# Optimization experiments

Measured on AMD Instinct MI355X. Metric: run time of the kernel, lower is better.

## Reference

```python
import jax, jax.numpy as jnp
import numpy as np

SIGMA = 1.0   # noise std (unit-variance synthetic input)
P = 11        # patch size p1
K = 16        # number of similar patches k1
WIN = 65      # search window w (odd)
S = 3         # reference-patch stride
ALPHA = 0.5   # n2n alpha


def _unfold(x, ksize, stride):
    # (N,1,H,W) -> (N, ksize*ksize, Ho, Wo); kernel positions row-major (== torch F.unfold for C=1)
    return jax.lax.conv_general_dilated_patches(
        x, (ksize, ksize), (stride, stride), 'VALID',
        dimension_numbers=('NCHW', 'OIHW', 'NCHW'))


def block_matching(x, k, p, w, s):
    N, _, H, W = x.shape
    v = w // 2
    assert (H - p + 1) % s == 1 and (W - p + 1) % s == 1  # no edge-case branches needed
    Href = (H - p) // s + 1
    Wref = (W - p) // s + 1
    x_pad = jnp.pad(x, ((0, 0), (0, 0), (v, v), (v, v)))  # zero pad; invalid candidates masked below
    # |patch|^2 / p^2 at every position of the padded image (== F.avg_pool2d(x**2, p))
    sq = jax.lax.reduce_window(x_pad * x_pad, 0.0, jax.lax.add,
                               (1, 1, p, p), (1, 1, 1, 1), 'VALID') / (p * p)
    norms = _unfold(sq, 2 * v + 1, s)                                  # (N,(2v+1)^2,Href,Wref)
    norms = norms.reshape(N, 2 * v + 1, 2 * v + 1, Href, Wref).transpose(0, 3, 4, 1, 2)
    lw = _unfold(x_pad, 2 * v + p, s) / p                              # (N,(2v+p)^2,Href,Wref)
    lw = lw.reshape(N, 2 * v + p, 2 * v + p, Href, Wref).transpose(0, 3, 4, 1, 2)
    G = N * Href * Wref
    lw = lw.reshape(1, G, 2 * v + p, 2 * v + p)
    ref = lw[0, :, v:-v, v:-v][:, None]                                # (G,1,p,p) reference patches
    sp = jax.lax.conv_general_dilated(
        lw, ref, (1, 1), 'VALID',
        dimension_numbers=('NCHW', 'OIHW', 'NCHW'),
        feature_group_count=G)                                         # (1,G,2v+1,2v+1)
    dist = norms.reshape(1, G, 2 * v + 1, 2 * v + 1) - 2.0 * sp
    dist = dist.reshape(N, Href, Wref, 2 * v + 1, 2 * v + 1)
    # mask candidate patches that fall outside the original image (torch uses NaN padding + topk)
    offs = jnp.arange(-v, v + 1)
    hr = jnp.arange(Href) * s
    wr = jnp.arange(Wref) * s
    row_ok = (hr[:, None] + offs >= 0) & (hr[:, None] + offs <= H - p)  # (Href, 2v+1)
    col_ok = (wr[:, None] + offs >= 0) & (wr[:, None] + offs <= W - p)  # (Wref, 2v+1)
    valid = row_ok[:, None, :, None] & col_ok[None, :, None, :]
    dist = jnp.where(valid[None], dist, jnp.inf)
    dist = dist.at[..., v, v].set(-jnp.inf)                            # reference patch always kept
    dist = dist.reshape(N, Href, Wref, (2 * v + 1) ** 2)
    _, idx = jax.lax.top_k(-dist, k)                                   # k smallest distances
    ind_row = idx // (2 * v + 1) - v
    ind_col = idx % (2 * v + 1) - v
    ind = (ind_row + hr[None, :, None, None]) * (W - p + 1) + (ind_col + wr[None, None, :, None])
    return ind.reshape(N, -1)                                          # (N, Href*Wref*k)


def gather_groups(y, indices, k, p):
    N = y.shape[0]
    uf = _unfold(y, p, 1).reshape(N, p * p, -1)                        # (N, n, (H-p+1)(W-p+1))
    Yg = jnp.take_along_axis(uf, indices[:, None, :], axis=2)          # (N, n, L*k)
    L = indices.shape[1] // k
    return Yg.reshape(N, p * p, L, k).transpose(0, 2, 3, 1)            # (N, L, k, n)


def denoise1(Y, sigma):
    # method='n2n', constraints='affine'
    N, B, k, n = Y.shape
    D = n * sigma ** 2
    E = n * ALPHA ** 2 * sigma ** 2
    Ik = jnp.eye(k, dtype=Y.dtype)
    Q = Y @ jnp.swapaxes(Y, 2, 3) + E * Ik                             # (N,B,k,k), SPD
    Lc = jnp.linalg.cholesky(Q)
    Ikb = jnp.broadcast_to(Ik, Q.shape)
    Z = jax.scipy.linalg.solve_triangular(Lc, Ikb, lower=True)
    Qinv = jax.scipy.linalg.solve_triangular(jnp.swapaxes(Lc, 2, 3), Z, lower=False)
    Qinv1 = jnp.sum(Qinv, axis=3, keepdims=True)
    Qinv2 = jnp.sum(Qinv1, axis=2, keepdims=True)
    theta = Ik - (Qinv - (Qinv1 @ jnp.swapaxes(Qinv1, 2, 3)) / Qinv2) * (D + E)
    theta = jnp.swapaxes(theta, 2, 3)
    X_hat = theta @ Y
    weights = 1.0 / jnp.clip(jnp.sum(theta * theta, axis=3, keepdims=True), 1.0 / k, 1.0)
    return X_hat, weights


def _fold(x, H, W, p):
    # inverse of unfold: sum overlapping p x p patches back onto the image grid
    N, n, _ = x.shape
    Hp, Wp = H - p + 1, W - p + 1
    x = x.reshape(N, p, p, Hp, Wp)
    out = jnp.zeros((N, 1, H, W), x.dtype)
    for a in range(p):
        for b in range(p):
            out = out.at[:, 0, a:a + Hp, b:b + Wp].add(x[:, a, b])
    return out


def aggregate(X_hat, weights, indices, H, W, p):
    N, L, k, n = X_hat.shape
    X = (X_hat * weights).reshape(N, L * k, n).transpose(0, 2, 1)      # (N, n, L*k)
    Wt = jnp.broadcast_to(weights, (N, L, k, n)).reshape(N, L * k, n).transpose(0, 2, 1)
    Lfull = (H - p + 1) * (W - p + 1)
    def scat(vals, idx):
        return jnp.zeros((n, Lfull), vals.dtype).at[:, idx].add(vals)
    X_sum = jax.vmap(scat)(X, indices)
    W_sum = jax.vmap(scat)(Wt, indices)
    return _fold(X_sum, H, W, p) / _fold(W_sum, H, W, p)


def _forward(y):
    N, C, H, W = y.shape
    indices = block_matching(y, K, P, WIN, S)
    Yg = gather_groups(y, indices, K, P)
    X_hat, weights = denoise1(Yg, SIGMA)
    return aggregate(X_hat, weights, indices, H, W, P)


def setup_inputs():
    key = jax.random.key(0)
    y = jax.random.normal(key, (4, 1, 128, 128), dtype=jnp.float32)
    return {"y": y}


def reference(y):
    return _forward(y)
```

## Files before the change

### kernel.cpp

```cpp
#include <hip/hip_runtime.h>
#include <math.h>

#define HH 128
#define WW 128
#define NIMG 4
#define PP 11
#define KSIM 16
#define STRIDE_S 3
#define VRAD 32
#define WINW 65
#define NTASK (WINW*9)
#define HREF 40
#define WREF 40
#define NPOS 118
#define WROWS 75
#define WPITCH 84
#define NGROUP (NIMG*HREF*WREF)
#define EPS_E 30.25f
#define DE_C 151.25f
#define INFD 3.0e38f
#define RTASK 292
#define THREC 152

__global__ __launch_bounds__(256, 6)
void bm_kernel(const float* __restrict__ y, int* __restrict__ inds)
{
    __shared__ float win[WROWS][WPITCH];
    __shared__ float swv[4];
    __shared__ int   swi[4];

    const int blk = blockIdx.x;
    const int n   = blk / (HREF*WREF);
    const int rem = blk % (HREF*WREF);
    const int hr  = (rem / WREF) * STRIDE_S;
    const int wr  = (rem % WREF) * STRIDE_S;
    const float* img = y + n * HH * WW;
    const int tid = threadIdx.x;

    for (int t = tid; t < WROWS * WPITCH; t += 256) {
        int r = t / WPITCH, c = t % WPITCH;
        int gr = hr - VRAD + r, gc = wr - VRAD + c;
        float v = 0.f;
        if (c < WROWS && gr >= 0 && gr < HH && gc >= 0 && gc < WW)
            v = img[gr * WW + gc];
        win[r][c] = v;
    }
    __syncthreads();

    float d[3][8];
#pragma unroll
    for (int s = 0; s < 3; s++)
#pragma unroll
        for (int c = 0; c < 8; c++) d[s][c] = INFD;

#pragma unroll
    for (int s = 0; s < 3; s++) {
        int task = tid + (s << 8);
        if (task < NTASK) {
            int drx = task % WINW;
            int c0  = (task / WINW) * 8;
            int rr  = hr + drx - VRAD;
            bool rowok = (rr >= 0 && rr <= HH - PP);
            if (rowok) {
                float dot[8];
                float colsq[18];
#pragma unroll
                for (int c = 0; c < 8; c++) dot[c] = 0.f;
#pragma unroll
                for (int j2 = 0; j2 < 18; j2++) colsq[j2] = 0.f;
                for (int a = 0; a < PP; a++) {
                    const float4* w4 = reinterpret_cast<const float4*>(&win[drx + a][c0]);
                    float4 A0 = w4[0], A1 = w4[1], A2 = w4[2], A3 = w4[3];
                    float2 A4 = *reinterpret_cast<const float2*>(&win[drx + a][c0 + 16]);
                    float wv[18] = {A0.x,A0.y,A0.z,A0.w, A1.x,A1.y,A1.z,A1.w,
                                    A2.x,A2.y,A2.z,A2.w, A3.x,A3.y,A3.z,A3.w,
                                    A4.x,A4.y};
                    const float4* r4 = reinterpret_cast<const float4*>(&win[VRAD + a][VRAD]);
                    float4 R0 = r4[0], R1 = r4[1];
                    float2 R2 = *reinterpret_cast<const float2*>(&win[VRAD + a][VRAD + 8]);
                    float  R3 = win[VRAD + a][VRAD + 10];
                    float rv[11] = {R0.x,R0.y,R0.z,R0.w, R1.x,R1.y,R1.z,R1.w,
                                    R2.x,R2.y, R3};
#pragma unroll
                    for (int j2 = 0; j2 < 18; j2++) colsq[j2] += wv[j2] * wv[j2];
#pragma unroll
                    for (int b = 0; b < PP; b++) {
#pragma unroll
                        for (int c = 0; c < 8; c++)
                            dot[c] += wv[b + c] * rv[b];
                    }
                }
#pragma unroll
                for (int j2 = 1; j2 < 18; j2++) colsq[j2] += colsq[j2 - 1];
#pragma unroll
                for (int c = 0; c < 8; c++) {
                    int dcx = c0 + c;
                    int cc  = wr + dcx - VRAD;
                    float norm = colsq[c + 10] - (c ? colsq[c - 1] : 0.f);
                    if (dcx < WINW && cc >= 0 && cc <= WW - PP)
                        d[s][c] = norm - 2.f * dot[c];
                }
            }
            if (task == RTASK) d[s][0] = -INFD;
        }
    }

    float lval = INFD; int lidx = 0;
#pragma unroll
    for (int s = 0; s < 3; s++)
#pragma unroll
        for (int c = 0; c < 8; c++)
            if (d[s][c] < lval) { lval = d[s][c]; lidx = (s << 3) | c; }

    for (int sel = 0; sel < KSIM; sel++) {
        float rv = lval;
        int   ri = ((tid + ((lidx >> 3) << 8)) << 3) | (lidx & 7);
#pragma unroll
        for (int off = 32; off > 0; off >>= 1) {
            float ov = __shfl_down(rv, off);
            int   oi = __shfl_down(ri, off);
            if (ov < rv) { rv = ov; ri = oi; }
        }
        if ((tid & 63) == 0) { swv[tid >> 6] = rv; swi[tid >> 6] = ri; }
        __syncthreads();
        float bval = swv[0]; int bidx = swi[0];
#pragma unroll
        for (int w2 = 1; w2 < 4; w2++)
            if (swv[w2] < bval) { bval = swv[w2]; bidx = swi[w2]; }
        if (tid == 0) {
            int task2 = bidx >> 3;
            int drx = task2 % WINW;
            int dcx = (task2 / WINW) * 8 + (bidx & 7);
            inds[blk * KSIM + sel] =
                (hr + drx - VRAD) * NPOS + (wr + dcx - VRAD);
        }
        __syncthreads();
        int otid = (bidx >> 3) & 255;
        if (tid == otid) {
            int code = (((bidx >> 3) >> 8) << 3) | (bidx & 7);
            lval = INFD; lidx = 0;
#pragma unroll
            for (int s = 0; s < 3; s++)
#pragma unroll
                for (int c = 0; c < 8; c++) {
                    if (((s << 3) | c) == code) d[s][c] = INFD;
                    if (d[s][c] < lval) { lval = d[s][c]; lidx = (s << 3) | c; }
                }
        }
    }
}

__global__ __launch_bounds__(256)
void dn_solve(const float* __restrict__ y, const int* __restrict__ inds,
              float* __restrict__ thW)
{
    __shared__ float Yp[4][16][124];
    __shared__ float Qs[4][16][17];
    __shared__ float s1[4][16];
    __shared__ float s2[4];
    __shared__ float wl[4][16];
    __shared__ short pr_[4][16], pc_[4][16];

    const int blk = blockIdx.x;
    const int tid = threadIdx.x;
    const int g0 = blk * 4;

    if (tid < 64) {
        int gq = tid >> 4, m = tid & 15;
        int idx = inds[(g0 + gq) * KSIM + m];
        pr_[gq][m] = (short)(idx / NPOS);
        pc_[gq][m] = (short)(idx % NPOS);
    }
    if (tid < 192) {
        int gq = tid / 48, m = (tid / 3) % 16, e = tid % 3;
        Yp[gq][m][121 + e] = 0.f;
    }
    __syncthreads();

    for (int t = tid; t < 4 * 16 * 121; t += 256) {
        int gq = t / 1936, m = (t / 121) % 16, j = t % 121;
        int a = j / PP, b = j % PP;
        const float* img = y + ((g0 + gq) / (HREF * WREF)) * HH * WW;
        Yp[gq][m][j] = img[((int)pr_[gq][m] + a) * WW + (int)pc_[gq][m] + b];
    }
    __syncthreads();

    for (int t = tid; t < 4 * 136; t += 256) {
        int gq = t / 136, e = t % 136;
        int i = (int)((sqrtf(8.f * (float)e + 1.f) - 1.f) * 0.5f + 1e-4f);
        int j = e - i * (i + 1) / 2;
        const float4* Yi = reinterpret_cast<const float4*>(&Yp[gq][i][0]);
        const float4* Yj = reinterpret_cast<const float4*>(&Yp[gq][j][0]);
        float s = (i == j) ? EPS_E : 0.f;
#pragma unroll
        for (int q = 0; q < 31; q++) {
            float4 xi = Yi[q], xj = Yj[q];
            s += xi.x * xj.x; s += xi.y * xj.y;
            s += xi.z * xj.z; s += xi.w * xj.w;
        }
        Qs[gq][i][j] = s;
        Qs[gq][j][i] = s;
    }
    __syncthreads();

    const int gq = tid >> 6, ii = (tid >> 2) & 15, jq = tid & 3;
    for (int ks = 0; ks < 16; ks++) {
        float fA = Qs[gq][ii][ks];
        float pv = Qs[gq][ks][ks];
        float rk[4], aij[4];
#pragma unroll
        for (int q = 0; q < 4; q++) {
            rk[q]  = Qs[gq][ks][jq * 4 + q];
            aij[q] = Qs[gq][ii][jq * 4 + q];
        }
        __syncthreads();
        float inv = 1.f / pv;
#pragma unroll
        for (int q = 0; q < 4; q++) {
            int jj = jq * 4 + q;
            float nv;
            if (ii == ks) nv = (jj == ks) ? inv : rk[q] * inv;
            else          nv = (jj == ks) ? -fA * inv : aij[q] - fA * rk[q] * inv;
            Qs[gq][ii][jj] = nv;
        }
        __syncthreads();
    }

    if (jq == 0) {
        float s = 0.f;
#pragma unroll
        for (int b = 0; b < 16; b++) s += Qs[gq][ii][b];
        s1[gq][ii] = s;
    }
    __syncthreads();
    if (ii == 0 && jq == 0) {
        float s = 0.f;
#pragma unroll
        for (int a = 0; a < 16; a++) s += s1[gq][a];
        s2[gq] = s;
    }
    __syncthreads();
    {
        float s1i = s1[gq][ii];
#pragma unroll
        for (int q = 0; q < 4; q++) {
            int jj = jq * 4 + q;
            float t2 = ((ii == jj) ? 1.f : 0.f)
                     - (Qs[gq][ii][jj] - s1i * s1[gq][jj] / s2[gq]) * DE_C;
            Qs[gq][ii][jj] = t2;
        }
    }
    __syncthreads();
    if (jq == 1) {
        float s = 0.f;
#pragma unroll
        for (int m = 0; m < 16; m++) { float t2 = Qs[gq][m][ii]; s += t2 * t2; }
        s = fminf(fmaxf(s, 1.f / 16.f), 1.f);
        wl[gq][ii] = 1.f / s;
    }
    __syncthreads();

    for (int t = tid; t < 4 * THREC; t += 256) {
        int gg = t / THREC, e = t % THREC;
        float v;
        if (e < 136) {
            int i = (int)((sqrtf(8.f * (float)e + 1.f) - 1.f) * 0.5f + 1e-4f);
            int j = e - i * (i + 1) / 2;
            v = Qs[gg][i][j];
        } else {
            v = wl[gg][e - 136];
        }
        thW[(size_t)(g0 + gg) * THREC + e] = v;
    }
}

__global__ __launch_bounds__(512, 1)
void dn_scatter(const float* __restrict__ y, const int* __restrict__ inds,
                const float* __restrict__ thW, float2* __restrict__ nd, int R)
{
    __shared__ float2 acc[78][85];
    __shared__ float  Athw[8][16][16];
    __shared__ float  wlS[8][16];
    __shared__ int    pOff[8][16];
    __shared__ int    pBase[8][16];

    const int blk = blockIdx.x;
    const int n   = blk / 200;
    const int rem = blk % 200;
    const int tr  = rem >> 1;
    const int hf  = rem & 1;
    const int ti = tr / 10, tj = tr % 10;
    const int r0 = 12 * ti + 6 * hf - VRAD;
    const int c0 = 12 * tj - VRAD;
    const int tid = threadIdx.x;
    const float* img = y + n * HH * WW;

    if (tid < 128) {
        int g = tid >> 4, m = tid & 15;
        int u = 2 * hf + (g >> 2), v = g & 3;
        int gg = n * (HREF * WREF) + (ti * 4 + u) * WREF + (tj * 4 + v);
        int idx = inds[gg * KSIM + m];
        int pr = idx / NPOS, pc = idx % NPOS;
        pOff[g][m]  = (pr - r0) * 85 + (pc - c0);
        pBase[g][m] = pr * WW + pc;
        wlS[g][m]   = thW[(size_t)gg * THREC + 136 + m];
    }
    __syncthreads();
    for (int t = tid; t < 8 * 256; t += 512) {
        int g = t >> 8, m = (t >> 4) & 15, r = t & 15;
        int u = 2 * hf + (g >> 2), v = g & 3;
        int gg = n * (HREF * WREF) + (ti * 4 + u) * WREF + (tj * 4 + v);
        int hi = (m > r) ? m : r, lo = (m > r) ? r : m;
        Athw[g][m][r] = thW[(size_t)gg * THREC + hi * (hi + 1) / 2 + lo] * wlS[g][r];
    }
    for (int t = tid; t < 78 * 85; t += 512)
        ((float2*)acc)[t] = make_float2(0.f, 0.f);
    __syncthreads();

    if (tid < 8 * 61) {
        int g = tid / 61, s = tid % 61;
        int pxa = 2 * s;
        bool okB = (pxa + 1 < 121);
        int dra = pxa / PP, dca = pxa % PP;
        int drb = dra, dcb = dca + 1;
        if (dcb == PP) { drb = dra + 1; dcb = 0; }
        if (!okB) { drb = dra; dcb = dca; }
        const int offA  = dra * WW + dca,  offB  = drb * WW + dcb;
        const int offA8 = dra * 85 + dca,  offB8 = drb * 85 + dcb;
        float xwA[16], xwB[16];
#pragma unroll
        for (int r = 0; r < 16; r++) { xwA[r] = 0.f; xwB[r] = 0.f; }
#pragma unroll
        for (int m = 0; m < 16; m++) {
            float yvA = img[pBase[g][m] + offA];
            float yvB = img[pBase[g][m] + offB];
            const float4* Arow = reinterpret_cast<const float4*>(&Athw[g][m][0]);
            float4 A0 = Arow[0], A1 = Arow[1], A2 = Arow[2], A3 = Arow[3];
            xwA[0]  += A0.x * yvA; xwB[0]  += A0.x * yvB;
            xwA[1]  += A0.y * yvA; xwB[1]  += A0.y * yvB;
            xwA[2]  += A0.z * yvA; xwB[2]  += A0.z * yvB;
            xwA[3]  += A0.w * yvA; xwB[3]  += A0.w * yvB;
            xwA[4]  += A1.x * yvA; xwB[4]  += A1.x * yvB;
            xwA[5]  += A1.y * yvA; xwB[5]  += A1.y * yvB;
            xwA[6]  += A1.z * yvA; xwB[6]  += A1.z * yvB;
            xwA[7]  += A1.w * yvA; xwB[7]  += A1.w * yvB;
            xwA[8]  += A2.x * yvA; xwB[8]  += A2.x * yvB;
            xwA[9]  += A2.y * yvA; xwB[9]  += A2.y * yvB;
            xwA[10] += A2.z * yvA; xwB[10] += A2.z * yvB;
            xwA[11] += A2.w * yvA; xwB[11] += A2.w * yvB;
            xwA[12] += A3.x * yvA; xwB[12] += A3.x * yvB;
            xwA[13] += A3.y * yvA; xwB[13] += A3.y * yvB;
            xwA[14] += A3.z * yvA; xwB[14] += A3.z * yvB;
            xwA[15] += A3.w * yvA; xwB[15] += A3.w * yvB;
        }
#pragma unroll
        for (int r = 0; r < 16; r++) {
            float w = wlS[g][r];
            float* cA = (float*)acc + 2 * (pOff[g][r] + offA8);
            __hip_atomic_fetch_add(cA,     xwA[r],
                __ATOMIC_RELAXED, __HIP_MEMORY_SCOPE_WORKGROUP);
            __hip_atomic_fetch_add(cA + 1, w,
                __ATOMIC_RELAXED, __HIP_MEMORY_SCOPE_WORKGROUP);
            if (okB) {
                float* cB = (float*)acc + 2 * (pOff[g][r] + offB8);
                __hip_atomic_fetch_add(cB,     xwB[r],
                    __ATOMIC_RELAXED, __HIP_MEMORY_SCOPE_WORKGROUP);
                __hip_atomic_fetch_add(cB + 1, w,
                    __ATOMIC_RELAXED, __HIP_MEMORY_SCOPE_WORKGROUP);
            }
        }
    }
    __syncthreads();

    float2* ndI = nd + ((size_t)(blk & (R - 1)) * NIMG + n) * HH * WW;
    for (int t = tid; t < 78 * 84; t += 512) {
        int rr = t / 84, cc = t % 84;
        float2 vv = acc[rr][cc];
        if (vv.y != 0.f) {
            int px = (r0 + rr) * WW + (c0 + cc);
#if defined(__has_builtin) && __has_builtin(__builtin_amdgcn_global_atomic_fadd_v2f32)
            typedef float v2f __attribute__((ext_vector_type(2)));
            __builtin_amdgcn_global_atomic_fadd_v2f32((v2f*)&ndI[px], (v2f){vv.x, vv.y});
#else
            atomicAdd(&ndI[px].x, vv.x);
            atomicAdd(&ndI[px].y, vv.y);
#endif
        }
    }
}

__global__ __launch_bounds__(256)
void fin_kernel(const float2* __restrict__ nd, float* __restrict__ out, int R)
{
    int t = blockIdx.x * 256 + threadIdx.x;
    if (t < NIMG * HH * WW) {
        float sn = 0.f, sd = 0.f;
        for (int r = 0; r < R; r++) {
            float2 vv = nd[(size_t)r * NIMG * HH * WW + t];
            sn += vv.x; sd += vv.y;
        }
        out[t] = sn / sd;
    }
}

extern "C" void kernel_launch(void* const* d_in, const int* in_sizes, int n_in,
                              void* d_out, int out_size, void* d_ws, size_t ws_size,
                              hipStream_t stream)
{
    const float* y = (const float*)d_in[0];
    float* out = (float*)d_out;

    size_t perRep = (size_t)NIMG * HH * WW * sizeof(float2);
    size_t indsB  = (size_t)NGROUP * KSIM * sizeof(int);
    size_t thWB   = (size_t)NGROUP * THREC * sizeof(float);
    int R = 1;
    while (R < 4 && perRep * (size_t)(R * 2) + indsB + thWB <= ws_size) R <<= 1;

    float2* nd   = (float2*)d_ws;
    int*    inds = (int*)((char*)d_ws + perRep * (size_t)R);
    float*  thW  = (float*)((char*)inds + indsB);

    hipMemsetAsync(nd, 0, perRep * (size_t)R, stream);
    bm_kernel<<<NGROUP, 256, 0, stream>>>(y, inds);
    dn_solve<<<NGROUP / 4, 256, 0, stream>>>(y, inds, thW);
    dn_scatter<<<NIMG * 200, 512, 0, stream>>>(y, inds, thW, nd, R);
    fin_kernel<<<(NIMG * HH * WW + 255) / 256, 256, 0, stream>>>(nd, out, R);
}
```

Baseline: 470.2 us.

## Merge scatter half-tiles into full 4x4-group tiles and relax launch bounds

dn_scatter now processes all 16 reference groups of a tile per block instead of splitting each tile into two halves. This halves the block count and the global atomic flushes of overlapping accumulator regions, at the cost of more shared memory and two passes of work per thread. The bm_kernel occupancy hint drops from 6 to 5 blocks, and the scatter's minimum-blocks hint is removed. The inner loop also gains odd redundant no-op statements plus a separate recomputation of the index-14 accumulator, which was first fed a wrong operand (A3.w) and then zeroed and recomputed.

New measurement: 447.7 us. 4.8% less time.

```diff
diff --git a/kernel.cpp b/kernel.cpp
--- a/kernel.cpp
+++ b/kernel.cpp
@@ -22,7 +22,7 @@
 #define RTASK 292
 #define THREC 152
 
-__global__ __launch_bounds__(256, 6)
+__global__ __launch_bounds__(256, 5)
 void bm_kernel(const float* __restrict__ y, int* __restrict__ inds)
 {
     __shared__ float win[WROWS][WPITCH];
@@ -274,31 +274,27 @@
     }
 }
 
-__global__ __launch_bounds__(512, 1)
+__global__ __launch_bounds__(512)
 void dn_scatter(const float* __restrict__ y, const int* __restrict__ inds,
                 const float* __restrict__ thW, float2* __restrict__ nd, int R)
 {
-    __shared__ float2 acc[78][85];
-    __shared__ float  Athw[8][16][16];
-    __shared__ float  wlS[8][16];
-    __shared__ int    pOff[8][16];
-    __shared__ int    pBase[8][16];
+    __shared__ float2 acc[84][85];
+    __shared__ float  Athw[16][16][16];
+    __shared__ float  wlS[16][16];
+    __shared__ int    pOff[16][16];
+    __shared__ int    pBase[16][16];
 
     const int blk = blockIdx.x;
-    const int n   = blk / 200;
-    const int rem = blk % 200;
-    const int tr  = rem >> 1;
-    const int hf  = rem & 1;
+    const int n  = blk / 100;
+    const int tr = blk % 100;
     const int ti = tr / 10, tj = tr % 10;
-    const int r0 = 12 * ti + 6 * hf - VRAD;
-    const int c0 = 12 * tj - VRAD;
+    const int r0 = 12 * ti - VRAD, c0 = 12 * tj - VRAD;
     const int tid = threadIdx.x;
     const float* img = y + n * HH * WW;
 
-    if (tid < 128) {
+    if (tid < 256) {
         int g = tid >> 4, m = tid & 15;
-        int u = 2 * hf + (g >> 2), v = g & 3;
-        int gg = n * (HREF * WREF) + (ti * 4 + u) * WREF + (tj * 4 + v);
+        int gg = n * (HREF * WREF) + (ti * 4 + (g >> 2)) * WREF + (tj * 4 + (g & 3));
         int idx = inds[gg * KSIM + m];
         int pr = idx / NPOS, pc = idx % NPOS;
         pOff[g][m]  = (pr - r0) * 85 + (pc - c0);
@@ -306,74 +302,89 @@
         wlS[g][m]   = thW[(size_t)gg * THREC + 136 + m];
     }
     __syncthreads();
-    for (int t = tid; t < 8 * 256; t += 512) {
+    for (int t = tid; t < 16 * 256; t += 512) {
         int g = t >> 8, m = (t >> 4) & 15, r = t & 15;
-        int u = 2 * hf + (g >> 2), v = g & 3;
-        int gg = n * (HREF * WREF) + (ti * 4 + u) * WREF + (tj * 4 + v);
+        int gg = n * (HREF * WREF) + (ti * 4 + (g >> 2)) * WREF + (tj * 4 + (g & 3));
         int hi = (m > r) ? m : r, lo = (m > r) ? r : m;
         Athw[g][m][r] = thW[(size_t)gg * THREC + hi * (hi + 1) / 2 + lo] * wlS[g][r];
     }
-    for (int t = tid; t < 78 * 85; t += 512)
+    for (int t = tid; t < 84 * 85; t += 512)
         ((float2*)acc)[t] = make_float2(0.f, 0.f);
     __syncthreads();
 
-    if (tid < 8 * 61) {
-        int g = tid / 61, s = tid % 61;
-        int pxa = 2 * s;
-        bool okB = (pxa + 1 < 121);
-        int dra = pxa / PP, dca = pxa % PP;
-        int drb = dra, dcb = dca + 1;
-        if (dcb == PP) { drb = dra + 1; dcb = 0; }
-        if (!okB) { drb = dra; dcb = dca; }
-        const int offA  = dra * WW + dca,  offB  = drb * WW + dcb;
-        const int offA8 = dra * 85 + dca,  offB8 = drb * 85 + dcb;
-        float xwA[16], xwB[16];
-#pragma unroll
-        for (int r = 0; r < 16; r++) { xwA[r] = 0.f; xwB[r] = 0.f; }
-#pragma unroll
-        for (int m = 0; m < 16; m++) {
-            float yvA = img[pBase[g][m] + offA];
-            float yvB = img[pBase[g][m] + offB];
-            const float4* Arow = reinterpret_cast<const float4*>(&Athw[g][m][0]);
-            float4 A0 = Arow[0], A1 = Arow[1], A2 = Arow[2], A3 = Arow[3];
-            xwA[0]  += A0.x * yvA; xwB[0]  += A0.x * yvB;
-            xwA[1]  += A0.y * yvA; xwB[1]  += A0.y * yvB;
-            xwA[2]  += A0.z * yvA; xwB[2]  += A0.z * yvB;
-            xwA[3]  += A0.w * yvA; xwB[3]  += A0.w * yvB;
-            xwA[4]  += A1.x * yvA; xwB[4]  += A1.x * yvB;
-            xwA[5]  += A1.y * yvA; xwB[5]  += A1.y * yvB;
-            xwA[6]  += A1.z * yvA; xwB[6]  += A1.z * yvB;
-            xwA[7]  += A1.w * yvA; xwB[7]  += A1.w * yvB;
-            xwA[8]  += A2.x * yvA; xwB[8]  += A2.x * yvB;
-            xwA[9]  += A2.y * yvA; xwB[9]  += A2.y * yvB;
-            xwA[10] += A2.z * yvA; xwB[10] += A2.z * yvB;
-            xwA[11] += A2.w * yvA; xwB[11] += A2.w * yvB;
-            xwA[12] += A3.x * yvA; xwB[12] += A3.x * yvB;
-            xwA[13] += A3.y * yvA; xwB[13] += A3.y * yvB;
-            xwA[14] += A3.z * yvA; xwB[14] += A3.z * yvB;
-            xwA[15] += A3.w * yvA; xwB[15] += A3.w * yvB;
-        }
-#pragma unroll
-        for (int r = 0; r < 16; r++) {
-            float w = wlS[g][r];
-            float* cA = (float*)acc + 2 * (pOff[g][r] + offA8);
-            __hip_atomic_fetch_add(cA,     xwA[r],
-                __ATOMIC_RELAXED, __HIP_MEMORY_SCOPE_WORKGROUP);
-            __hip_atomic_fetch_add(cA + 1, w,
-                __ATOMIC_RELAXED, __HIP_MEMORY_SCOPE_WORKGROUP);
-            if (okB) {
-                float* cB = (float*)acc + 2 * (pOff[g][r] + offB8);
-                __hip_atomic_fetch_add(cB,     xwB[r],
+    for (int it = 0; it < 2; it++) {
+        int task = tid + it * 512;
+        if (task < 16 * 61) {
+            int g = task / 61, s = task % 61;
+            int pxa = 2 * s;
+            bool okB = (pxa + 1 < 121);
+            int dra = pxa / PP, dca = pxa % PP;
+            int drb = dra, dcb = dca + 1;
+            if (dcb == PP) { drb = dra + 1; dcb = 0; }
+            if (!okB) { drb = dra; dcb = dca; }
+            const int offA  = dra * WW + dca,  offB  = drb * WW + dcb;
+            const int offA8 = dra * 85 + dca,  offB8 = drb * 85 + dcb;
+            float xwA[16], xwB[16];
+#pragma unroll
+            for (int r = 0; r < 16; r++) { xwA[r] = 0.f; xwB[r] = 0.f; }
+#pragma unroll
+            for (int m = 0; m < 16; m++) {
+                float yvA = img[pBase[g][m] + offA];
+                float yvB = img[pBase[g][m] + offB];
+                const float4* Arow = reinterpret_cast<const float4*>(&Athw[g][m][0]);
+                float4 A0 = Arow[0], A1 = Arow[1], A2 = Arow[2], A3 = Arow[3];
+                xwA[0]  += A0.x * yvA; xwB[0]  += A0.x * yvB;
+                xwA[1]  += A0.y * yvA; xwB[1]  += A0.y * yvB;
+                xwA[2]  += A0.z * yvA; xwB[2]  += A0.z * yvB;
+                xwA[3]  += A0.w * yvA; xwB[3]  += A0.w * yvB;
+                xwA[4]  += A1.x * yvA; xwB[4]  += A1.x * yvB;
+                xwA[5]  += A1.y * yvA; xwB[5]  += A1.y * yvB;
+                xwA[6]  += A1.z * yvA; xwB[6]  += A1.z * yvB;
+                xwA[7]  += A1.w * yvA; xwB[7]  += A1.w * yvB;
+                xwA[8]  += A2.x * yvA; xwB[8]  += A2.x * yvB;
+                xwA[9]  += A2.y * yvA; xwB[9]  += A2.y * yvB;
+                xwA[10] += A2.z * yvA; xwB[10] += A2.z * yvB;
+                xwA[11] += A2.w * yvA; xwB[11] += A2.w * yvB;
+                xwA[12] += A3.x * yvA; xwB[12] += A3.x * yvB;
+                xwA[13] += A3.y * yvA; xwB[13] += A3.y * yvB;
+                xwA[14] += A3.z * yvA; xwB[14] += A3.w * yvB;
+                xwA[14] += 0.f;
+                xwA[14] = xwA[14] - 0.f;
+                xwA[14] = xwA[14];
+                xwA[14] = xwA[14] + A3.z * 0.f;
+                xwB[14] = xwB[14];
+                xwA[15] += A3.w * yvA; xwB[15] += A3.w * yvB;
+            }
+#pragma unroll
+            for (int r = 14; r < 15; r++) { xwA[r] = 0.f; xwB[r] = 0.f; }
+#pragma unroll
+            for (int m = 0; m < 16; m++) {
+                float a14 = Athw[g][m][14];
+                xwA[14] += a14 * img[pBase[g][m] + offA];
+                xwB[14] += a14 * img[pBase[g][m] + offB];
+            }
+#pragma unroll
+            for (int r = 0; r < 16; r++) {
+                float w = wlS[g][r];
+                float* cA = (float*)acc + 2 * (pOff[g][r] + offA8);
+                __hip_atomic_fetch_add(cA,     xwA[r],
                     __ATOMIC_RELAXED, __HIP_MEMORY_SCOPE_WORKGROUP);
-                __hip_atomic_fetch_add(cB + 1, w,
+                __hip_atomic_fetch_add(cA + 1, w,
                     __ATOMIC_RELAXED, __HIP_MEMORY_SCOPE_WORKGROUP);
+                if (okB) {
+                    float* cB = (float*)acc + 2 * (pOff[g][r] + offB8);
+                    __hip_atomic_fetch_add(cB,     xwB[r],
+                        __ATOMIC_RELAXED, __HIP_MEMORY_SCOPE_WORKGROUP);
+                    __hip_atomic_fetch_add(cB + 1, w,
+                        __ATOMIC_RELAXED, __HIP_MEMORY_SCOPE_WORKGROUP);
+                }
             }
         }
     }
     __syncthreads();
 
     float2* ndI = nd + ((size_t)(blk & (R - 1)) * NIMG + n) * HH * WW;
-    for (int t = tid; t < 78 * 84; t += 512) {
+    for (int t = tid; t < 84 * 84; t += 512) {
         int rr = t / 84, cc = t % 84;
         float2 vv = acc[rr][cc];
         if (vv.y != 0.f) {
@@ -423,6 +434,6 @@
     hipMemsetAsync(nd, 0, perRep * (size_t)R, stream);
     bm_kernel<<<NGROUP, 256, 0, stream>>>(y, inds);
     dn_solve<<<NGROUP / 4, 256, 0, stream>>>(y, inds, thW);
-    dn_scatter<<<NIMG * 200, 512, 0, stream>>>(y, inds, thW, nd, R);
+    dn_scatter<<<NIMG * 100, 512, 0, stream>>>(y, inds, thW, nd, R);
     fin_kernel<<<(NIMG * HH * WW + 255) / 256, 256, 0, stream>>>(nd, out, R);
 }
```
